# Kernel optimization log

Measured on AMD Instinct MI355X. Metric: run time of the kernel, lower is better.

The kernel has to match this reference:

```python
import jax, jax.numpy as jnp
import numpy as np

COLB = 16            # COL_BLOCK_WIDTH
IN_W = 1024          # input_width; zero_inputs=0 so input_locations = arange(IN_W)
OUT_W = 512          # output_width
DEPTH = 8            # network_depth
IN_L = 4             # butterfly_in_depth
OUT_L = 4            # butterfly_out_depth
ACT = 8              # activations_per_block
BLOCKS = 64          # blocks_per_layer -> num_inputs = 1024 per module
CURV = 1.0
GROW = BLOCKS * ACT  # 512 new rows per module
TOTAL = IN_W + DEPTH * GROW  # 5120
BATCH = 4096


def setup_inputs() -> dict:
    key = jax.random.key(0)
    k1, k2, k3 = jax.random.split(key, 3)
    input_data = jax.random.normal(k1, (IN_W, BATCH), dtype=jnp.float32)
    scales = jnp.full((IN_W,), 0.05, dtype=jnp.float32)
    # angles uniform in (-pi, pi), shape [depth, in_layers+out_layers, num_inputs/2]
    angles = (jax.random.uniform(k2, (DEPTH, IN_L + OUT_L, BLOCKS * COLB // 2)) * 2.0 - 1.0) * np.pi
    angles = angles.astype(jnp.float32)
    biases = jax.random.normal(k3, (DEPTH, GROW), dtype=jnp.float32) * 0.05
    # per-module indices_in = randperm(total_width_so_far)[:num_inputs]
    rng = np.random.RandomState(0)
    tw = IN_W
    idxs = []
    for _ in range(DEPTH):
        idxs.append(rng.permutation(tw)[: BLOCKS * COLB].astype(np.int32))
        tw += GROW
    indices_in = jnp.asarray(np.stack(idxs))  # [depth, 1024]
    return {"input_data": input_data, "scales": scales, "angles": angles,
            "biases": biases, "indices_in": indices_in}


def _rotate(x, ang, stride):
    # x: [W, B]; pair row i (with (i//stride)%2==0) with row i+stride inside 16-blocks
    W, B = x.shape
    xr = x.reshape(W // (2 * stride), 2, stride, B)
    a = ang.reshape(W // (2 * stride), stride)[:, :, None]
    c, s = jnp.cos(a), jnp.sin(a)
    lo, hi = xr[:, 0], xr[:, 1]              # [W/2s, s, B]
    nlo = c * lo + s * hi
    nhi = -s * lo + c * hi
    return jnp.stack([nlo, nhi], axis=1).reshape(W, B)


def _butterfly_module(data, ang, bias, idx, idx_out):
    W = BLOCKS * COLB
    x = data[idx]                             # gather [1024, B]
    for l in range(IN_L):
        x = _rotate(x, ang[l], 2 ** (l % 4))
    xb = x.reshape(BLOCKS, COLB, -1)
    pre = xb[:, :ACT, :] + bias.reshape(BLOCKS, ACT)[:, :, None]
    # curvature (smoothed-ReLU) activation
    act = 0.5 * (pre + jnp.sqrt(pre * pre + CURV * CURV))
    xb = xb.at[:, :ACT, :].set(act)
    x = xb.reshape(W, -1)
    for l in range(OUT_L):
        x = _rotate(x, ang[IN_L + l], 2 ** ((IN_L + l) % 4))
    data = data.at[idx].set(x)                # scatter working set back
    data = data.at[idx_out: idx_out + GROW].set(act.reshape(GROW, -1))
    return data


def reference(input_data, scales, angles, biases, indices_in):
    B = input_data.shape[1]
    data = jnp.zeros((TOTAL, B), dtype=input_data.dtype)
    data = data.at[:IN_W].set(scales[:, None] * input_data)
    for i in range(DEPTH):
        data = _butterfly_module(data, angles[i], biases[i], indices_in[i], IN_W + GROW * i)
    return data[TOTAL - OUT_W:]
```

## Files before the change

kernel.cpp:

```cpp
#include <hip/hip_runtime.h>
#include <math.h>

#define N_INW   1024
#define N_DEPTH 8
#define N_GROW  512
#define N_BATCH 4096
#define N_ROWS  4608
#define COLSTR  9220
#define LDS_B   (16 * COLSTR)
#define MAT_B   ((size_t)N_DEPTH * 64 * 2 * 512)
#define ADR_OFF MAT_B
#define WS_NEED (MAT_B + (size_t)N_DEPTH * 1024 * 2)

typedef __attribute__((ext_vector_type(4))) _Float16 h4;
typedef __attribute__((ext_vector_type(4))) float    f4;
typedef __attribute__((ext_vector_type(2))) unsigned u32x2;

#define PKU(x, y) __builtin_bit_cast(unsigned int,                             \
                      __builtin_amdgcn_cvt_pkrtz((x), (y)))

__global__ void precompute_kernel(const float* __restrict__ angles,
                                  const int*   __restrict__ indices,
                                  char* __restrict__ ws) {
    int id = blockIdx.x * blockDim.x + threadIdx.x;
    if (id < 16384) {
        int k = id & 15, b = (id >> 4) & 63, half = (id >> 10) & 1, m = id >> 11;
        float v[16];
#pragma unroll
        for (int i = 0; i < 16; ++i) v[i] = (i == k) ? 1.f : 0.f;
#pragma unroll
        for (int lp = 0; lp < 4; ++lp) {
            int s = 1 << lp;
            const float* ab = angles + m * 4096 + (half * 4 + lp) * 512 + b * 8;
#pragma unroll
            for (int p = 0; p < 8; ++p) {
                int q = p >> lp, r = p & (s - 1);
                int lo = q * 2 * s + r, hi = lo + s;
                float a = ab[p], c, sn;
                __sincosf(a, &sn, &c);
                float nl = c * v[lo] + sn * v[hi];
                float nh = c * v[hi] - sn * v[lo];
                v[lo] = nl; v[hi] = nh;
            }
        }
        char* rec = ws + (((size_t)(m * 64 + b) * 2 + half) << 9);
#pragma unroll
        for (int row = 0; row < 16; ++row) {
            int lane = ((k >> 2) << 4) | row;
            *(unsigned short*)(rec + lane * 8 + (k & 3) * 2) =
                __builtin_bit_cast(unsigned short, (_Float16)v[row]);
        }
    }
    if (id < 8192) {
        ((unsigned short*)(ws + ADR_OFF))[id] =
            (unsigned short)(indices[(id >> 10) * N_INW + (id & 1023)] << 1);
    }
}

__device__ __forceinline__ float actf(float x) {
    return 0.5f * (x + __builtin_amdgcn_sqrtf(x * x + 1.0f));
}

#define DECLSET(P) h4 P##ai[8], P##ao[8]; u32x2 P##ad[8];

#define LOADSET(P, M) do {                                                     \
    _Pragma("unroll")                                                          \
    for (int bb = 0; bb < 8; ++bb) {                                           \
        const char* rb = mats + (((size_t)((M) * 64 + wblk0 + bb) * 2) << 9);  \
        P##ai[bb] = *(const h4*)(rb + lane * 8);                               \
        P##ao[bb] = *(const h4*)(rb + 512 + lane * 8);                         \
        P##ad[bb] = *(const u32x2*)(adr + ((M) * 64 + wblk0 + bb) * 16 + (q << 2)); \
    } } while (0)

#define PROC(P, NP, M, LAST) do {                                              \
  if (!(LAST)) LOADSET(NP, (M) + 1);                                           \
  u32x2 bw[8];                                                                 \
  _Pragma("unroll")                                                            \
  for (int bb = 0; bb < 8; ++bb) {                                             \
    u32x2 ad = P##ad[bb];                                                      \
    unsigned g0 = *(const unsigned short*)(L + cB + (ad.x & 0xffffu));         \
    unsigned g1 = *(const unsigned short*)(L + cB + (ad.x >> 16));             \
    unsigned g2 = *(const unsigned short*)(L + cB + (ad.y & 0xffffu));         \
    unsigned g3 = *(const unsigned short*)(L + cB + (ad.y >> 16));             \
    bw[bb].x = g0 | (g1 << 16); bw[bb].y = g2 | (g3 << 16);                    \
  }                                                                            \
  _Pragma("unroll")                                                            \
  for (int bb = 0; bb < 8; ++bb) {                                             \
    const int blk = wblk0 + bb;                                                \
    f4 cin = f4zero;                                                           \
    if (q < 2)                                                                 \
        cin = *(const f4*)(biases + (M) * N_GROW + blk * 8 + ((q & 1) << 2));  \
    f4 d = __builtin_amdgcn_mfma_f32_16x16x16f16(                              \
               P##ai[bb], __builtin_bit_cast(h4, bw[bb]), cin, 0, 0, 0);       \
    if (q < 2) {                                                               \
        d.x = actf(d.x); d.y = actf(d.y); d.z = actf(d.z); d.w = actf(d.w);    \
    }                                                                          \
    if (LAST) {                                                                \
        if (q < 2) {                                                           \
            float* op = out + (size_t)(blk * 8 + (q << 2)) * N_BATCH + cg + c; \
            op[0] = d.x; op[N_BATCH] = d.y;                                    \
            op[2 * N_BATCH] = d.z; op[3 * N_BATCH] = d.w;                      \
        }                                                                      \
    } else {                                                                   \
        unsigned p0 = PKU(d.x, d.y), p1 = PKU(d.z, d.w);                       \
        if (q < 2) {                      \
            char* ap = L + cB +                                                \
                ((N_INW + (M) * N_GROW + blk * 8 + (q << 2)) << 1);            \
            *(unsigned*)ap = p0; *(unsigned*)(ap + 4) = p1;                    \
        }                                                                      \
        u32x2 bp; bp.x = p0; bp.y = p1;                                        \
        f4 d2 = __builtin_amdgcn_mfma_f32_16x16x16f16(                         \
                    P##ao[bb], __builtin_bit_cast(h4, bp), f4zero, 0, 0, 0);   \
        u32x2 ad = P##ad[bb];                                                  \
        *(unsigned short*)(L + cB + (ad.x & 0xffffu)) =                        \
            __builtin_bit_cast(unsigned short, (_Float16)d2.x);                \
        *(unsigned short*)(L + cB + (ad.x >> 16)) =                            \
            __builtin_bit_cast(unsigned short, (_Float16)d2.y);                \
        *(unsigned short*)(L + cB + (ad.y & 0xffffu)) =                        \
            __builtin_bit_cast(unsigned short, (_Float16)d2.z);                \
        *(unsigned short*)(L + cB + (ad.y >> 16)) =                            \
            __builtin_bit_cast(unsigned short, (_Float16)d2.w);                \
    }                                                                          \
  }                                                                            \
  if (!(LAST)) __syncthreads();                                                \
} while (0)

__global__ __launch_bounds__(512, 2)
void butterfly_mfma_kernel(const float* __restrict__ input,
                           const float* __restrict__ scales,
                           const float* __restrict__ biases,
                           const char*  __restrict__ mats,
                           const unsigned short* __restrict__ adr,
                           float* __restrict__ out) {
    extern __shared__ char L[];
    const int t = threadIdx.x, lane = t & 63, w = t >> 6;
    const int c = lane & 15, q = lane >> 4;
    const int cB = c * COLSTR;
    const int wblk0 = w * 8;
    const int cg = blockIdx.x * 16;
    const f4 f4zero = {0.f, 0.f, 0.f, 0.f};

    DECLSET(A) DECLSET(B)
    LOADSET(A, 0);

    {
        const int rg = (t >> 4) * 32;
        const int ci = t & 15;
#pragma unroll
        for (int i = 0; i < 32; i += 2) {
            int r = rg + i;
            float v0 = input[(size_t)r * N_BATCH + cg + ci] * scales[r];
            float v1 = input[(size_t)(r + 1) * N_BATCH + cg + ci] * scales[r + 1];
            *(unsigned*)(L + ci * COLSTR + (r << 1)) = PKU(v0, v1);
        }
    }
    __syncthreads();

#pragma unroll 1
    for (int tt = 0; tt < 3; ++tt) {
        PROC(A, B, 2 * tt, 0);
        PROC(B, A, 2 * tt + 1, 0);
    }
    PROC(A, B, 6, 0);
    PROC(B, B, 7, 1);
}

extern "C" void kernel_launch(void* const* d_in, const int* in_sizes, int n_in,
                              void* d_out, int out_size, void* d_ws, size_t ws_size,
                              hipStream_t stream) {
    const float* input   = (const float*)d_in[0];
    const float* scales  = (const float*)d_in[1];
    const float* angles  = (const float*)d_in[2];
    const float* biases  = (const float*)d_in[3];
    const int*   indices = (const int*)d_in[4];
    float* out = (float*)d_out;

    precompute_kernel<<<64, 256, 0, stream>>>(angles, indices, (char*)d_ws);
    butterfly_mfma_kernel<<<256, 512, LDS_B, stream>>>(
        input, scales, biases, (const char*)d_ws,
        (const unsigned short*)((char*)d_ws + ADR_OFF), out);
}
```

Measured before the change: 104.7 us.

## Interleave matrix records, widen address table, add setprio, vectorize input staging

Stores the in and out rotation matrices for each block interleaved, so one 16-byte load per lane fetches both. Widens the gather address table to 32-bit entries, which removes the mask and shift unpacking at the cost of twice the table size and more registers. Wraps the MFMA phase in s_setprio to favour the compute waves. Rewrites the input staging loop to load float2 pairs along the batch dimension.

```diff
diff --git a/kernel.cpp b/kernel.cpp
--- a/kernel.cpp
+++ b/kernel.cpp
@@ -5,18 +5,17 @@
 #define N_DEPTH 8
 #define N_GROW  512
 #define N_BATCH 4096
-#define N_ROWS  4608
 #define COLSTR  9220
 #define LDS_B   (16 * COLSTR)
-#define MAT_B   ((size_t)N_DEPTH * 64 * 2 * 512)
+#define MAT_B   ((size_t)N_DEPTH * 64 * 1024)
 #define ADR_OFF MAT_B
-#define WS_NEED (MAT_B + (size_t)N_DEPTH * 1024 * 2)
 
 typedef __attribute__((ext_vector_type(4))) _Float16 h4;
 typedef __attribute__((ext_vector_type(4))) float    f4;
-typedef __attribute__((ext_vector_type(2))) unsigned u32x2;
+typedef __attribute__((ext_vector_type(2))) float    F2;
+typedef __attribute__((ext_vector_type(2))) unsigned u2;
 
-#define PKU(x, y) __builtin_bit_cast(unsigned int,                             \
+#define PKU(x, y) __builtin_bit_cast(unsigned,                                 \
                       __builtin_amdgcn_cvt_pkrtz((x), (y)))
 
 __global__ void precompute_kernel(const float* __restrict__ angles,
@@ -34,8 +33,8 @@
             const float* ab = angles + m * 4096 + (half * 4 + lp) * 512 + b * 8;
 #pragma unroll
             for (int p = 0; p < 8; ++p) {
-                int q = p >> lp, r = p & (s - 1);
-                int lo = q * 2 * s + r, hi = lo + s;
+                int qq = p >> lp, r = p & (s - 1);
+                int lo = qq * 2 * s + r, hi = lo + s;
                 float a = ab[p], c, sn;
                 __sincosf(a, &sn, &c);
                 float nl = c * v[lo] + sn * v[hi];
@@ -43,17 +42,17 @@
                 v[lo] = nl; v[hi] = nh;
             }
         }
-        char* rec = ws + (((size_t)(m * 64 + b) * 2 + half) << 9);
+        char* rec = ws + ((size_t)(m * 64 + b) << 10);
 #pragma unroll
         for (int row = 0; row < 16; ++row) {
             int lane = ((k >> 2) << 4) | row;
-            *(unsigned short*)(rec + lane * 8 + (k & 3) * 2) =
+            *(unsigned short*)(rec + lane * 16 + half * 8 + (k & 3) * 2) =
                 __builtin_bit_cast(unsigned short, (_Float16)v[row]);
         }
     }
     if (id < 8192) {
-        ((unsigned short*)(ws + ADR_OFF))[id] =
-            (unsigned short)(indices[(id >> 10) * N_INW + (id & 1023)] << 1);
+        ((unsigned*)(ws + ADR_OFF))[id] =
+            (unsigned)(indices[(id >> 10) * N_INW + (id & 1023)] << 1);
     }
 }
 
@@ -61,29 +60,33 @@
     return 0.5f * (x + __builtin_amdgcn_sqrtf(x * x + 1.0f));
 }
 
-#define DECLSET(P) h4 P##ai[8], P##ao[8]; u32x2 P##ad[8];
+#define DECLSET(P) h4 P##ai[8], P##ao[8]; uint4 P##ad[8];
 
 #define LOADSET(P, M) do {                                                     \
     _Pragma("unroll")                                                          \
     for (int bb = 0; bb < 8; ++bb) {                                           \
-        const char* rb = mats + (((size_t)((M) * 64 + wblk0 + bb) * 2) << 9);  \
-        P##ai[bb] = *(const h4*)(rb + lane * 8);                               \
-        P##ao[bb] = *(const h4*)(rb + 512 + lane * 8);                         \
-        P##ad[bb] = *(const u32x2*)(adr + ((M) * 64 + wblk0 + bb) * 16 + (q << 2)); \
+        const int rb = (M) * 64 + wblk0 + bb;                                  \
+        uint4 rc = *(const uint4*)(mats + ((size_t)rb << 10) + (lane << 4));   \
+        u2 t0; t0.x = rc.x; t0.y = rc.y;                                       \
+        u2 t1; t1.x = rc.z; t1.y = rc.w;                                       \
+        P##ai[bb] = __builtin_bit_cast(h4, t0);                                \
+        P##ao[bb] = __builtin_bit_cast(h4, t1);                                \
+        P##ad[bb] = *(const uint4*)(adr + (size_t)rb * 64 + (q << 4));         \
     } } while (0)
 
 #define PROC(P, NP, M, LAST) do {                                              \
   if (!(LAST)) LOADSET(NP, (M) + 1);                                           \
-  u32x2 bw[8];                                                                 \
+  u2 bw[8];                                                                    \
   _Pragma("unroll")                                                            \
   for (int bb = 0; bb < 8; ++bb) {                                             \
-    u32x2 ad = P##ad[bb];                                                      \
-    unsigned g0 = *(const unsigned short*)(L + cB + (ad.x & 0xffffu));         \
-    unsigned g1 = *(const unsigned short*)(L + cB + (ad.x >> 16));             \
-    unsigned g2 = *(const unsigned short*)(L + cB + (ad.y & 0xffffu));         \
-    unsigned g3 = *(const unsigned short*)(L + cB + (ad.y >> 16));             \
+    uint4 ad = P##ad[bb];                                                      \
+    unsigned g0 = *(const unsigned short*)(L + cB + ad.x);                     \
+    unsigned g1 = *(const unsigned short*)(L + cB + ad.y);                     \
+    unsigned g2 = *(const unsigned short*)(L + cB + ad.z);                     \
+    unsigned g3 = *(const unsigned short*)(L + cB + ad.w);                     \
     bw[bb].x = g0 | (g1 << 16); bw[bb].y = g2 | (g3 << 16);                    \
   }                                                                            \
+  __builtin_amdgcn_s_setprio(1);                                               \
   _Pragma("unroll")                                                            \
   for (int bb = 0; bb < 8; ++bb) {                                             \
     const int blk = wblk0 + bb;                                                \
@@ -103,25 +106,26 @@
         }                                                                      \
     } else {                                                                   \
         unsigned p0 = PKU(d.x, d.y), p1 = PKU(d.z, d.w);                       \
-        if (q < 2) {                      \
+        if (q < 2) {     \
             char* ap = L + cB +                                                \
                 ((N_INW + (M) * N_GROW + blk * 8 + (q << 2)) << 1);            \
             *(unsigned*)ap = p0; *(unsigned*)(ap + 4) = p1;                    \
         }                                                                      \
-        u32x2 bp; bp.x = p0; bp.y = p1;                                        \
+        u2 bp; bp.x = p0; bp.y = p1;                                           \
         f4 d2 = __builtin_amdgcn_mfma_f32_16x16x16f16(                         \
                     P##ao[bb], __builtin_bit_cast(h4, bp), f4zero, 0, 0, 0);   \
-        u32x2 ad = P##ad[bb];                                                  \
-        *(unsigned short*)(L + cB + (ad.x & 0xffffu)) =                        \
+        uint4 ad = P##ad[bb];                                                  \
+        *(unsigned short*)(L + cB + ad.x) =                                    \
             __builtin_bit_cast(unsigned short, (_Float16)d2.x);                \
-        *(unsigned short*)(L + cB + (ad.x >> 16)) =                            \
+        *(unsigned short*)(L + cB + ad.y) =                                    \
             __builtin_bit_cast(unsigned short, (_Float16)d2.y);                \
-        *(unsigned short*)(L + cB + (ad.y & 0xffffu)) =                        \
+        *(unsigned short*)(L + cB + ad.z) =                                    \
             __builtin_bit_cast(unsigned short, (_Float16)d2.z);                \
-        *(unsigned short*)(L + cB + (ad.y >> 16)) =                            \
+        *(unsigned short*)(L + cB + ad.w) =                                    \
             __builtin_bit_cast(unsigned short, (_Float16)d2.w);                \
     }                                                                          \
   }                                                                            \
+  __builtin_amdgcn_s_setprio(0);                                               \
   if (!(LAST)) __syncthreads();                                                \
 } while (0)
 
@@ -130,7 +134,7 @@
                            const float* __restrict__ scales,
                            const float* __restrict__ biases,
                            const char*  __restrict__ mats,
-                           const unsigned short* __restrict__ adr,
+                           const char*  __restrict__ adr,
                            float* __restrict__ out) {
     extern __shared__ char L[];
     const int t = threadIdx.x, lane = t & 63, w = t >> 6;
@@ -144,14 +148,16 @@
     LOADSET(A, 0);
 
     {
-        const int rg = (t >> 4) * 32;
-        const int ci = t & 15;
+        const int cp = (t & 7) << 1;
+        const int r0 = (t >> 3) << 4;
 #pragma unroll
-        for (int i = 0; i < 32; i += 2) {
-            int r = rg + i;
-            float v0 = input[(size_t)r * N_BATCH + cg + ci] * scales[r];
-            float v1 = input[(size_t)(r + 1) * N_BATCH + cg + ci] * scales[r + 1];
-            *(unsigned*)(L + ci * COLSTR + (r << 1)) = PKU(v0, v1);
+        for (int i = 0; i < 16; i += 2) {
+            int r = r0 + i;
+            F2 w0 = *(const F2*)(input + (size_t)r * N_BATCH + cg + cp);
+            F2 w1 = *(const F2*)(input + (size_t)(r + 1) * N_BATCH + cg + cp);
+            F2 sc = *(const F2*)(scales + r);
+            *(unsigned*)(L + cp * COLSTR + (r << 1))       = PKU(sc.x * w0.x, sc.y * w1.x);
+            *(unsigned*)(L + (cp + 1) * COLSTR + (r << 1)) = PKU(sc.x * w0.y, sc.y * w1.y);
         }
     }
     __syncthreads();
@@ -178,5 +184,5 @@
     precompute_kernel<<<64, 256, 0, stream>>>(angles, indices, (char*)d_ws);
     butterfly_mfma_kernel<<<256, 512, LDS_B, stream>>>(
         input, scales, biases, (const char*)d_ws,
-        (const unsigned short*)((char*)d_ws + ADR_OFF), out);
+        (const char*)d_ws + ADR_OFF, out);
 }
```

Result: no change. 102.7 us (-2.0%).
